# Kernel optimization log

Hardware: AMD Instinct MI355X
Metric: run time of the kernel (lower is better)

Reference implementation:

```python
import math
import jax, jax.numpy as jnp
import numpy as np


def setup_inputs() -> dict:
    key = jax.random.key(0)
    ks = jax.random.split(key, 6)
    b, t, e, h = 4, 1024, 512, 8
    x = jax.random.normal(ks[0], (b, t, e), dtype=jnp.float32)
    s = 0.02  # small init scale to keep logits sane
    Wq = jax.random.normal(ks[1], (e, e * h), dtype=jnp.float32) * s
    Wk = jax.random.normal(ks[2], (e, e * h), dtype=jnp.float32) * s
    Wv = jax.random.normal(ks[3], (e, e * h), dtype=jnp.float32) * s
    Wo = jax.random.normal(ks[4], (e * h, e), dtype=jnp.float32) * s
    bo = jnp.zeros((e,), dtype=jnp.float32)
    return {"x": x, "Wq": Wq, "Wk": Wk, "Wv": Wv, "Wo": Wo, "bo": bo}


def reference(x, Wq, Wk, Wv, Wo, bo):
    b, t, e = x.shape
    h = Wq.shape[1] // e  # wide attention: each head uses full emb dim
    # project and split heads -> (b, h, t, e)
    q = (x @ Wq).reshape(b, t, h, e).transpose(0, 2, 1, 3)
    k = (x @ Wk).reshape(b, t, h, e).transpose(0, 2, 1, 3)
    v = (x @ Wv).reshape(b, t, h, e).transpose(0, 2, 1, 3)
    q = q / math.sqrt(e)
    dot = jnp.einsum("bhqe,bhke->bhqk", q, k)  # (b, h, t, t)
    # causal mask: positions j > i get -inf (mask_diagonal=False -> offset=1)
    causal = jnp.tril(jnp.ones((t, t), dtype=bool))
    dot = jnp.where(causal[None, None], dot, -jnp.inf)
    att = jax.nn.softmax(dot, axis=-1)
    out = jnp.einsum("bhqk,bhke->bhqe", att, v)
    out = out.transpose(0, 2, 1, 3).reshape(b, t, h * e)
    return out @ Wo + bo
```

## Files before the change

kernel.cpp:

```cpp
#include <hip/hip_runtime.h>
#include <hip/hip_bf16.h>

typedef unsigned short u16;
typedef __attribute__((ext_vector_type(4))) float f32x4;
typedef __attribute__((ext_vector_type(8))) short s16x8;
typedef __attribute__((ext_vector_type(4))) short s16x4;

#define DEVFN static __device__ __forceinline__

DEVFN u16 f2bf(float f) {
  unsigned u = __float_as_uint(f);
  return (u16)((u + 0x7fffu + ((u >> 16) & 1u)) >> 16);
}
DEVFN float bf2f(u16 h) { return __uint_as_float(((unsigned)h) << 16); }

DEVFN void gl_lds16(const void* g, void* l) {
  __builtin_amdgcn_global_load_lds(
      (const __attribute__((address_space(1))) unsigned int*)g,
      (__attribute__((address_space(3))) unsigned int*)l, 16, 0, 0);
}

DEVFN f32x4 mfma16(s16x8 a, s16x8 b, f32x4 c) {
  return __builtin_amdgcn_mfma_f32_16x16x32_bf16(a, b, c, 0, 0, 0);
}

__global__ void k_cvt4(const float4* __restrict__ x, const float4* __restrict__ Wq,
                       const float4* __restrict__ Wk, const float4* __restrict__ Wv,
                       u16* __restrict__ dst, float qscale, int n4) {
  const int z = blockIdx.y;
  const float4* src = (z == 0) ? x : (z == 1) ? Wq : (z == 2) ? Wk : Wv;
  const float scale = (z == 1) ? qscale : 1.f;
  u16* d = (z == 0) ? dst : dst + 2097152 + (size_t)z * 2097152;
  int i = blockIdx.x * 256 + threadIdx.x;
  if (i >= n4) return;
  float4 v = src[i];
  s16x4 o;
  o[0] = (short)f2bf(v.x * scale); o[1] = (short)f2bf(v.y * scale);
  o[2] = (short)f2bf(v.z * scale); o[3] = (short)f2bf(v.w * scale);
  *(s16x4*)(d + (size_t)i * 4) = o;
}

__global__ void k_transpose_w(const float* __restrict__ src, u16* __restrict__ dst,
                              int K, int N) {
  __shared__ float tile[64][65];
  int k0 = blockIdx.x * 64, n0 = blockIdx.y * 64;
  int t = threadIdx.x, c = t & 63, r4 = t >> 6;
#pragma unroll
  for (int i = 0; i < 16; ++i) {
    int r = i * 4 + r4;
    tile[r][c] = src[(size_t)(k0 + r) * N + n0 + c];
  }
  __syncthreads();
#pragma unroll
  for (int i = 0; i < 16; ++i) {
    int r = i * 4 + r4;
    dst[(size_t)(n0 + r) * K + k0 + c] = f2bf(tile[c][r]);
  }
}

__global__ void k_transpose_x(const u16* __restrict__ xb, u16* __restrict__ xT) {
  __shared__ u16 tile[64][65];
  const int bz = blockIdx.z;
  const int r0 = blockIdx.x * 64, c0 = blockIdx.y * 64;
  int t = threadIdx.x, c = t & 63, r4 = t >> 6;
#pragma unroll
  for (int i = 0; i < 16; ++i) {
    int r = i * 4 + r4;
    tile[r][c] = xb[(size_t)(bz * 1024 + r0 + r) * 512 + c0 + c];
  }
  __syncthreads();
#pragma unroll
  for (int i = 0; i < 16; ++i) {
    int r = i * 4 + r4;
    xT[(size_t)bz * 524288 + (size_t)(c0 + r) * 1024 + r0 + c] = tile[c][r];
  }
}

template <int BM, int BN, int EPI, int CAUSAL, int VARK>
__global__ void __launch_bounds__(256) k_gemm(
    const u16* __restrict__ A, const u16* __restrict__ Bt,
    void* __restrict__ Cp, const float* __restrict__ bias,
    int K, int lda, int ldb, int ldc,
    size_t sAb, size_t sAh, size_t sBb, size_t sBh, size_t sCb, size_t sCh) {
  const unsigned nx = gridDim.x, ny = gridDim.y;
  const unsigned nwg = nx * ny * gridDim.z;
  const unsigned L = blockIdx.x + nx * (blockIdx.y + ny * blockIdx.z);
  const unsigned o = (nwg & 7) ? L : ((L & 7) * (nwg >> 3) + (L >> 3));
  const unsigned bx = o % nx, o2 = o / nx;
  const unsigned by = o2 % ny, bz = o2 / ny;

  if (CAUSAL && bx > by) return;
  constexpr int MR = BM / 32, NR = BN / 32;
  constexpr int LPT = (BM + BN) / 64;
  constexpr int ABUF = BM * 32, BBUF = BN * 32;
  __shared__ alignas(16) u16 Alds[3 * ABUF];
  __shared__ alignas(16) u16 Blds[3 * BBUF];
  const int tid = threadIdx.x, lane = tid & 63, wv = tid >> 6;
  const int wr = wv >> 1, wc = wv & 1;
  const int row0 = by * BM, col0 = bx * BN;
  const int zb = bz >> 3, zh = bz & 7;
  const char* Ab = (const char*)(A + (size_t)zb * sAb + (size_t)zh * sAh);
  const char* Bb = (const char*)(Bt + (size_t)zb * sBb + (size_t)zh * sBh);
  const size_t coff = (size_t)zb * sCb + (size_t)zh * sCh;
  const int Klim = VARK ? (by + 1) * BM : K;
  const int ntiles = Klim >> 5;
  const f32x4 zero4 = {0.f, 0.f, 0.f, 0.f};

  const int scb = (((lane & 3) ^ ((lane >> 3) & 3))) * 16;
  auto stage = [&](int buf, int k0) {
    char* abase = (char*)(Alds + buf * ABUF);
    char* bbase = (char*)(Blds + buf * BBUF);
#pragma unroll
    for (int j = 0; j < BM / 64; ++j) {
      int ch = j * 4 + wv;
      int r = ch * 16 + (lane >> 2);
      gl_lds16(Ab + ((size_t)(row0 + r) * lda + k0) * 2 + scb, abase + ch * 1024);
    }
#pragma unroll
    for (int j = 0; j < BN / 64; ++j) {
      int ch = j * 4 + wv;
      int r = ch * 16 + (lane >> 2);
      gl_lds16(Bb + ((size_t)(col0 + r) * ldb + k0) * 2 + scb, bbase + ch * 1024);
    }
  };

  f32x4 acc[MR][NR];
#pragma unroll
  for (int m = 0; m < MR; ++m)
#pragma unroll
    for (int n = 0; n < NR; ++n) acc[m][n] = zero4;

  stage(0, 0);
  if (ntiles > 1) stage(1, 32);

  const int rcb = (((lane >> 4) ^ ((lane >> 1) & 3)) & 3) * 16;

  int t = 0;
  for (int k0 = 0; k0 < Klim; k0 += 32, ++t) {
    if (t + 1 < ntiles)
      asm volatile("s_waitcnt vmcnt(%0)" :: "i"(LPT) : "memory");
    else
      asm volatile("s_waitcnt vmcnt(0)" ::: "memory");
    __builtin_amdgcn_s_barrier();
    asm volatile("" ::: "memory");
    if (t + 2 < ntiles) stage((t + 2) % 3, k0 + 64);
    const char* abase = (const char*)(Alds + (t % 3) * ABUF);
    const char* bbase = (const char*)(Blds + (t % 3) * BBUF);
    s16x8 af[MR], bfr[NR];
#pragma unroll
    for (int m = 0; m < MR; ++m)
      af[m] = *(const s16x8*)(abase +
               (wr * (BM / 2) + m * 16 + (lane & 15)) * 64 + rcb);
#pragma unroll
    for (int n = 0; n < NR; ++n)
      bfr[n] = *(const s16x8*)(bbase +
                (wc * (BN / 2) + n * 16 + (lane & 15)) * 64 + rcb);
    __builtin_amdgcn_s_setprio(1);
#pragma unroll
    for (int m = 0; m < MR; ++m)
#pragma unroll
      for (int n = 0; n < NR; ++n) acc[m][n] = mfma16(af[m], bfr[n], acc[m][n]);
    __builtin_amdgcn_s_setprio(0);
  }
#pragma unroll
  for (int m = 0; m < MR; ++m)
#pragma unroll
    for (int n = 0; n < NR; ++n)
#pragma unroll
      for (int i = 0; i < 4; ++i) {
        int r = row0 + wr * (BM / 2) + m * 16 + (lane >> 4) * 4 + i;
        int c = col0 + wc * (BN / 2) + n * 16 + (lane & 15);
        if (EPI == 0)
          ((u16*)Cp)[coff + (size_t)r * ldc + c] = f2bf(acc[m][n][i]);
        else if (EPI == 1)
          ((float*)Cp)[coff + (size_t)r * ldc + c] = acc[m][n][i] + bias[c];
        else
          ((float*)Cp)[coff + (size_t)r * ldc + c] = acc[m][n][i];
      }
}

__global__ void __launch_bounds__(256) k_softmax(u16* __restrict__ S) {
  const int tid = threadIdx.x, lane = tid & 63, w = tid >> 6;
  const int row = blockIdx.x * 4 + w;
  const int q = row & 1023;
  u16* rowp = S + (size_t)(row >> 10) * 1048576 + (size_t)q * 1024;
  const int c0 = lane * 8, c1 = 512 + lane * 8;
  const bool hi = (q >= 512);
  s16x8 v0 = *(const s16x8*)(rowp + c0);
  s16x8 v1 = {};
  if (hi) v1 = *(const s16x8*)(rowp + c1);
  float f[16];
#pragma unroll
  for (int j = 0; j < 8; ++j) {
    f[j]     = (c0 + j <= q)       ? bf2f((u16)v0[j]) : -3e38f;
    f[8 + j] = (hi && c1 + j <= q) ? bf2f((u16)v1[j]) : -3e38f;
  }
  float m = f[0];
#pragma unroll
  for (int j = 1; j < 16; ++j) m = fmaxf(m, f[j]);
  m = fmaxf(m, __shfl_xor(m, 1));
  m = fmaxf(m, __shfl_xor(m, 2));
  m = fmaxf(m, __shfl_xor(m, 4));
  m = fmaxf(m, __shfl_xor(m, 8));
  m = fmaxf(m, __shfl_xor(m, 16));
  m = fmaxf(m, __shfl_xor(m, 32));
  float sum = 0.f;
#pragma unroll
  for (int j = 0; j < 16; ++j) { f[j] = __expf(f[j] - m); sum += f[j]; }
  sum += __shfl_xor(sum, 1);
  sum += __shfl_xor(sum, 2);
  sum += __shfl_xor(sum, 4);
  sum += __shfl_xor(sum, 8);
  sum += __shfl_xor(sum, 16);
  sum += __shfl_xor(sum, 32);
  const float inv = 1.f / sum;
#pragma unroll
  for (int j = 0; j < 8; ++j) {
    v0[j] = (short)f2bf(f[j] * inv);
    v1[j] = (short)f2bf(f[8 + j] * inv);
  }
  *(s16x8*)(rowp + c0) = v0;
  if (hi) *(s16x8*)(rowp + c1) = v1;
}

__global__ void k_reduce2(const float4* __restrict__ P, const float4* __restrict__ bias,
                          float4* __restrict__ out, int n4) {
  int i = blockIdx.x * 256 + threadIdx.x;
  if (i >= n4) return;
  float4 a = P[i], b = P[i + 524288];
  float4 bb = bias[i & 127];
  float4 o;
  o.x = a.x + b.x + bb.x;
  o.y = a.y + b.y + bb.y;
  o.z = a.z + b.z + bb.z;
  o.w = a.w + b.w + bb.w;
  out[i] = o;
}

extern "C" void kernel_launch(void* const* d_in, const int* in_sizes, int n_in,
                              void* d_out, int out_size, void* d_ws, size_t ws_size,
                              hipStream_t stream) {
  (void)in_sizes; (void)n_in; (void)out_size; (void)ws_size;
  const float* x  = (const float*)d_in[0];
  const float* Wq = (const float*)d_in[1];
  const float* Wk = (const float*)d_in[2];
  const float* Wv = (const float*)d_in[3];
  const float* Wo = (const float*)d_in[4];
  const float* bo = (const float*)d_in[5];
  float* out = (float*)d_out;

  u16* ws   = (u16*)d_ws;
  u16* xb   = ws;
  u16* xT   = ws + 2097152;
  u16* Wqb  = ws + 4194304;
  u16* Wkb  = ws + 6291456;
  u16* Wvb  = ws + 8388608;
  u16* WoT  = ws + 10485760;
  u16* G    = ws + 12582912;
  u16* WvoT = ws + 14680064;
  u16* y    = ws + 16777216;
  u16* S    = ws + 33554432;
  u16* Z    = ws + 67108864;
  float* Pp = (float*)(ws + 16777216);

  const float qscale = 0.044194173824159216f;

  k_cvt4<<<dim3(2048, 4), 256, 0, stream>>>((const float4*)x, (const float4*)Wq,
                                            (const float4*)Wk, (const float4*)Wv,
                                            ws, qscale, 524288);
  k_transpose_w<<<dim3(64, 8), 256, 0, stream>>>(Wo, WoT, 4096, 512);
  k_transpose_x<<<dim3(16, 8, 4), 256, 0, stream>>>(xb, xT);

  k_gemm<64, 64, 0, 0, 0><<<dim3(8, 8, 8), 256, 0, stream>>>(
      Wkb, Wqb, (void*)G, nullptr, 512, 4096, 4096, 512,
      0, 512, 0, 512, 0, 262144);
  k_gemm<64, 64, 0, 0, 0><<<dim3(8, 8, 8), 256, 0, stream>>>(
      WoT, Wvb, (void*)WvoT, nullptr, 512, 4096, 4096, 4096,
      0, 512, 0, 512, 0, 512);

  k_gemm<128, 128, 0, 0, 0><<<dim3(4, 32, 8), 256, 0, stream>>>(
      xb, G, (void*)y, nullptr, 512, 512, 512, 512,
      0, 0, 0, 262144, 0, 2097152);

  k_gemm<128, 128, 0, 1, 0><<<dim3(8, 8, 32), 256, 0, stream>>>(
      y, xb, (void*)S, nullptr, 512, 512, 512, 1024,
      524288, 2097152, 524288, 0, 8388608, 1048576);

  k_softmax<<<8192, 256, 0, stream>>>(S);

  k_gemm<128, 128, 0, 0, 1><<<dim3(4, 8, 32), 256, 0, stream>>>(
      S, xT, (void*)Z, nullptr, 1024, 1024, 1024, 4096,
      8388608, 1048576, 524288, 0, 4194304, 512);

  k_gemm<128, 64, 2, 0, 0><<<dim3(8, 32, 2), 256, 0, stream>>>(
      Z, WvoT, (void*)Pp, nullptr, 2048, 4096, 4096, 512,
      0, 2048, 0, 2048, 0, 2097152);
  k_reduce2<<<2048, 256, 0, stream>>>((const float4*)Pp, (const float4*)bo,
                                      (float4*)out, 524288);
}
```

Baseline: 193.6 us.

## Use 256x128 triple-buffered GEMM kernel and split-K by 8 for output projection

Adds a new GEMM kernel with 256x128 tiles, 512 threads, a three-stage LDS ring buffer with a swizzled layout, a grid remap that groups workgroups in strides of eight, and raised priority around the MFMA block. The four main GEMMs switch to it. The output projection now splits K eight ways instead of two, and a new reduce kernel sums the eight partials plus the bias. The aim is more data reuse per tile and better overlap of loads with compute, at the cost of larger tiles that can waste work on the causal and variable-K GEMMs, plus extra partial-sum traffic.

```diff
diff --git a/kernel.cpp b/kernel.cpp
--- a/kernel.cpp
+++ b/kernel.cpp
@@ -179,6 +179,109 @@
       }
 }
 
+template <int EPI, int CAUSAL, int VARK>
+__global__ void __launch_bounds__(512, 2) k_gemm2(
+    const u16* __restrict__ A, const u16* __restrict__ Bt,
+    void* __restrict__ Cp, const float* __restrict__ bias,
+    int K, int lda, int ldb, int ldc,
+    size_t sAb, size_t sAh, size_t sBb, size_t sBh, size_t sCb, size_t sCh) {
+  constexpr int BM = 256, BN = 128, MR = 4, NR = 4;
+  constexpr int LPT = 3;
+  constexpr int ABUF = BM * 32, BBUF = BN * 32;
+  const unsigned nx = gridDim.x, ny = gridDim.y;
+  const unsigned nwg = nx * ny * gridDim.z;
+  const unsigned L = blockIdx.x + nx * (blockIdx.y + ny * blockIdx.z);
+  const unsigned o = (nwg & 7) ? L : ((L & 7) * (nwg >> 3) + (L >> 3));
+  const unsigned bx = o % nx, o2 = o / nx;
+  const unsigned by = o2 % ny, bz = o2 / ny;
+
+  const int row0 = by * BM, col0 = bx * BN;
+  if (CAUSAL && col0 >= row0 + BM) return;
+  __shared__ alignas(16) u16 Alds[3 * ABUF];
+  __shared__ alignas(16) u16 Blds[3 * BBUF];
+  const int tid = threadIdx.x, lane = tid & 63, wv = tid >> 6;
+  const int wr = wv >> 1, wc = wv & 1;
+  const int zb = bz >> 3, zh = bz & 7;
+  const char* Ab = (const char*)(A + (size_t)zb * sAb + (size_t)zh * sAh);
+  const char* Bb = (const char*)(Bt + (size_t)zb * sBb + (size_t)zh * sBh);
+  const size_t coff = (size_t)zb * sCb + (size_t)zh * sCh;
+  const int Klim = VARK ? (row0 + BM) : K;
+  const int ntiles = Klim >> 5;
+  const f32x4 zero4 = {0.f, 0.f, 0.f, 0.f};
+
+  const int scb = (((lane & 3) ^ ((lane >> 3) & 3))) * 16;
+  auto stage = [&](int buf, int k0) {
+    char* abase = (char*)(Alds + buf * ABUF);
+    char* bbase = (char*)(Blds + buf * BBUF);
+#pragma unroll
+    for (int j = 0; j < 3; ++j) {
+      int ch = wv * 3 + j;
+      if (ch < 16) {
+        int r = ch * 16 + (lane >> 2);
+        gl_lds16(Ab + ((size_t)(row0 + r) * lda + k0) * 2 + scb, abase + ch * 1024);
+      } else {
+        int r = (ch - 16) * 16 + (lane >> 2);
+        gl_lds16(Bb + ((size_t)(col0 + r) * ldb + k0) * 2 + scb,
+                 bbase + (ch - 16) * 1024);
+      }
+    }
+  };
+
+  f32x4 acc[MR][NR];
+#pragma unroll
+  for (int m = 0; m < MR; ++m)
+#pragma unroll
+    for (int n = 0; n < NR; ++n) acc[m][n] = zero4;
+
+  stage(0, 0);
+  if (ntiles > 1) stage(1, 32);
+
+  const int rcb = (((lane >> 4) ^ ((lane >> 1) & 3)) & 3) * 16;
+
+  int t = 0;
+  for (int k0 = 0; k0 < Klim; k0 += 32, ++t) {
+    if (t + 1 < ntiles)
+      asm volatile("s_waitcnt vmcnt(%0)" :: "i"(LPT) : "memory");
+    else
+      asm volatile("s_waitcnt vmcnt(0)" ::: "memory");
+    __builtin_amdgcn_s_barrier();
+    asm volatile("" ::: "memory");
+    if (t + 2 < ntiles) stage((t + 2) % 3, k0 + 64);
+    const char* abase = (const char*)(Alds + (t % 3) * ABUF);
+    const char* bbase = (const char*)(Blds + (t % 3) * BBUF);
+    s16x8 af[MR], bfr[NR];
+#pragma unroll
+    for (int m = 0; m < MR; ++m)
+      af[m] = *(const s16x8*)(abase +
+               (wr * 64 + m * 16 + (lane & 15)) * 64 + rcb);
+#pragma unroll
+    for (int n = 0; n < NR; ++n)
+      bfr[n] = *(const s16x8*)(bbase +
+                (wc * 64 + n * 16 + (lane & 15)) * 64 + rcb);
+    __builtin_amdgcn_s_setprio(1);
+#pragma unroll
+    for (int m = 0; m < MR; ++m)
+#pragma unroll
+      for (int n = 0; n < NR; ++n) acc[m][n] = mfma16(af[m], bfr[n], acc[m][n]);
+    __builtin_amdgcn_s_setprio(0);
+  }
+#pragma unroll
+  for (int m = 0; m < MR; ++m)
+#pragma unroll
+    for (int n = 0; n < NR; ++n)
+#pragma unroll
+      for (int i = 0; i < 4; ++i) {
+        int r = row0 + wr * 64 + m * 16 + (lane >> 4) * 4 + i;
+        int c = col0 + wc * 64 + n * 16 + (lane & 15);
+        if (EPI == 0)
+          ((u16*)Cp)[coff + (size_t)r * ldc + c] = f2bf(acc[m][n][i]);
+        else if (EPI == 1)
+          ((float*)Cp)[coff + (size_t)r * ldc + c] = acc[m][n][i] + bias[c];
+        else
+          ((float*)Cp)[coff + (size_t)r * ldc + c] = acc[m][n][i];
+      }
+}
+
 __global__ void __launch_bounds__(256) k_softmax(u16* __restrict__ S) {
   const int tid = threadIdx.x, lane = tid & 63, w = tid >> 6;
   const int row = blockIdx.x * 4 + w;
@@ -223,18 +326,20 @@
   if (hi) *(s16x8*)(rowp + c1) = v1;
 }
 
-__global__ void k_reduce2(const float4* __restrict__ P, const float4* __restrict__ bias,
+__global__ void k_reduce8(const float4* __restrict__ P, const float4* __restrict__ bias,
                           float4* __restrict__ out, int n4) {
   int i = blockIdx.x * 256 + threadIdx.x;
   if (i >= n4) return;
-  float4 a = P[i], b = P[i + 524288];
   float4 bb = bias[i & 127];
-  float4 o;
-  o.x = a.x + b.x + bb.x;
-  o.y = a.y + b.y + bb.y;
-  o.z = a.z + b.z + bb.z;
-  o.w = a.w + b.w + bb.w;
-  out[i] = o;
+  float sx = bb.x, sy = bb.y, sz = bb.z, sw = bb.w;
+#pragma unroll
+  for (int j = 0; j < 8; ++j) {
+    float4 a = P[i + (size_t)j * 524288];
+    sx += a.x; sy += a.y; sz += a.z; sw += a.w;
+  }
+  float4 o2;
+  o2.x = sx; o2.y = sy; o2.z = sz; o2.w = sw;
+  out[i] = o2;
 }
 
 extern "C" void kernel_launch(void* const* d_in, const int* in_sizes, int n_in,
@@ -261,7 +366,7 @@
   u16* y    = ws + 16777216;
   u16* S    = ws + 33554432;
   u16* Z    = ws + 67108864;
-  float* Pp = (float*)(ws + 16777216);
+  float* Pp = (float*)(ws + 33554432);
 
   const float qscale = 0.044194173824159216f;
 
@@ -278,23 +383,23 @@
       WoT, Wvb, (void*)WvoT, nullptr, 512, 4096, 4096, 4096,
       0, 512, 0, 512, 0, 512);
 
-  k_gemm<128, 128, 0, 0, 0><<<dim3(4, 32, 8), 256, 0, stream>>>(
+  k_gemm2<0, 0, 0><<<dim3(4, 16, 8), 512, 0, stream>>>(
       xb, G, (void*)y, nullptr, 512, 512, 512, 512,
       0, 0, 0, 262144, 0, 2097152);
 
-  k_gemm<128, 128, 0, 1, 0><<<dim3(8, 8, 32), 256, 0, stream>>>(
+  k_gemm2<0, 1, 0><<<dim3(8, 4, 32), 512, 0, stream>>>(
       y, xb, (void*)S, nullptr, 512, 512, 512, 1024,
       524288, 2097152, 524288, 0, 8388608, 1048576);
 
   k_softmax<<<8192, 256, 0, stream>>>(S);
 
-  k_gemm<128, 128, 0, 0, 1><<<dim3(4, 8, 32), 256, 0, stream>>>(
+  k_gemm2<0, 0, 1><<<dim3(4, 4, 32), 512, 0, stream>>>(
       S, xT, (void*)Z, nullptr, 1024, 1024, 1024, 4096,
       8388608, 1048576, 524288, 0, 4194304, 512);
 
-  k_gemm<128, 64, 2, 0, 0><<<dim3(8, 32, 2), 256, 0, stream>>>(
-      Z, WvoT, (void*)Pp, nullptr, 2048, 4096, 4096, 512,
-      0, 2048, 0, 2048, 0, 2097152);
-  k_reduce2<<<2048, 256, 0, stream>>>((const float4*)Pp, (const float4*)bo,
+  k_gemm2<2, 0, 0><<<dim3(4, 16, 8), 512, 0, stream>>>(
+      Z, WvoT, (void*)Pp, nullptr, 512, 4096, 4096, 512,
+      0, 512, 0, 512, 0, 2097152);
+  k_reduce8<<<2048, 256, 0, stream>>>((const float4*)Pp, (const float4*)bo,
                                       (float4*)out, 524288);
 }
```

Result: faster. 188.8 us (-2.4%).
